# Kernel optimization log

Hardware: AMD Instinct MI355X
Metric: run time of the kernel (lower is better)

## Reference

```python
import jax, jax.numpy as jnp
import numpy as np

D_MODEL = 4096
D_FF = 11008

def setup_inputs() -> dict:
    key = jax.random.key(0)
    k1, k2, k3, k4 = jax.random.split(key, 4)
    x = jax.random.normal(k1, (2, 2048, D_MODEL), dtype=jnp.float32)
    # Linear weights stored torch-style as [out_features, in_features]
    W_gate = jax.random.normal(k2, (D_FF, D_MODEL), dtype=jnp.float32) * (D_MODEL ** -0.5)
    W_up = jax.random.normal(k3, (D_FF, D_MODEL), dtype=jnp.float32) * (D_MODEL ** -0.5)
    W_down = jax.random.normal(k4, (D_MODEL, D_FF), dtype=jnp.float32) * (D_FF ** -0.5)
    return {"x": x, "W_gate": W_gate, "W_up": W_up, "W_down": W_down}

def reference(x, W_gate, W_up, W_down):
    out_shape = x.shape[:-1] + (W_down.shape[0],)
    xf = x.reshape(-1, x.shape[-1])                      # [T, d_model]
    up = jnp.einsum('td,fd->tf', xf, W_up)               # [T, d_ff]
    gate = jax.nn.silu(jnp.einsum('td,fd->tf', xf, W_gate))  # fused SiLU on gate proj
    h = gate * up                                        # [T, d_ff]
    y = jnp.einsum('tf,df->td', h, W_down)               # [T, d_model]
    return y.reshape(out_shape)
```

## Files before the change

kernel.cpp:

```cpp
#include <hip/hip_runtime.h>
#include <hip/hip_bf16.h>

#define D_MODEL 4096
#define D_FF    11008
#define NTOK    4096

typedef __attribute__((ext_vector_type(8))) short short8;
typedef __attribute__((ext_vector_type(4))) float f32x4;

__global__ void k_cvt(const float* __restrict__ in, __hip_bfloat16* __restrict__ out, int n8) {
    int i = blockIdx.x * blockDim.x + threadIdx.x;
    if (i >= n8) return;
    const float4* p = (const float4*)in;
    float4 v0 = p[(size_t)i * 2];
    float4 v1 = p[(size_t)i * 2 + 1];
    float vals[8] = {v0.x, v0.y, v0.z, v0.w, v1.x, v1.y, v1.z, v1.w};
    short8 o;
#pragma unroll
    for (int j = 0; j < 8; ++j) {
        __hip_bfloat16 b = __float2bfloat16(vals[j]);
        o[j] = *reinterpret_cast<short*>(&b);
    }
    *reinterpret_cast<short8*>(out + (size_t)i * 8) = o;
}

static __device__ __forceinline__ void stage_half(
    const __hip_bfloat16* g, int ld, __hip_bfloat16* lds, int tid)
{
#pragma unroll
    for (int s = 0; s < 2; ++s) {
        int ci = s * 512 + tid;
        int r  = ci >> 3;
        int c  = (ci & 7) ^ (r & 7);
        __builtin_amdgcn_global_load_lds(
            (const __attribute__((address_space(1))) void*)(g + (long)r * ld + c * 8),
            (__attribute__((address_space(3))) void*)(lds + ci * 8),
            16, 0, 0);
    }
}

static __device__ __forceinline__ int sw_off(int row, int kb) {
    return row * 64 + ((((kb >> 3) ^ (row & 7))) << 3);
}

#define GEMM_PHASE(cA, cB, IQ, LOADB, STAGE, VMC)                              \
    {                                                                          \
        short8 af[2][2];                                                       \
        _Pragma("unroll")                                                      \
        for (int ii = 0; ii < 2; ++ii)                                         \
            _Pragma("unroll")                                                  \
            for (int kk = 0; kk < 2; ++kk)                                     \
                af[ii][kk] = *reinterpret_cast<const short8*>(                 \
                    &(cA)[sw_off(wm * 128 + ((IQ) * 2 + ii) * 16 + r16,        \
                                 kk * 32 + g4 * 8)]);                          \
        if (LOADB) {                                                           \
            _Pragma("unroll")                                                  \
            for (int kk = 0; kk < 2; ++kk)                                     \
                _Pragma("unroll")                                              \
                for (int j = 0; j < 4; ++j)                                    \
                    bfr[kk][j] = *reinterpret_cast<const short8*>(             \
                        &(cB)[sw_off(wn * 64 + j * 16 + r16,                   \
                                     kk * 32 + g4 * 8)]);                      \
        }                                                                      \
        STAGE;                                                                 \
        VMC;                                                                   \
        __builtin_amdgcn_s_barrier();                                          \
        asm volatile("s_waitcnt lgkmcnt(0)" ::: "memory");                     \
        __builtin_amdgcn_sched_barrier(0);                                     \
        __builtin_amdgcn_s_setprio(1);                                         \
        _Pragma("unroll")                                                      \
        for (int ii = 0; ii < 2; ++ii)                                         \
            _Pragma("unroll")                                                  \
            for (int j = 0; j < 4; ++j) {                                      \
                acc[(IQ) * 2 + ii][j] = __builtin_amdgcn_mfma_f32_16x16x32_bf16( \
                    af[ii][0], bfr[0][j], acc[(IQ) * 2 + ii][j], 0, 0, 0);     \
                acc[(IQ) * 2 + ii][j] = __builtin_amdgcn_mfma_f32_16x16x32_bf16( \
                    af[ii][1], bfr[1][j], acc[(IQ) * 2 + ii][j], 0, 0, 0);     \
            }                                                                  \
        __builtin_amdgcn_s_setprio(0);                                         \
        __builtin_amdgcn_sched_barrier(0);                                     \
        __builtin_amdgcn_s_barrier();                                          \
    }

#define VM4 do { if (pf) asm volatile("s_waitcnt vmcnt(4)" ::: "memory");      \
                 else    asm volatile("s_waitcnt vmcnt(0)" ::: "memory"); } while (0)
#define VMNONE do {} while (0)

template<int EPI>
__global__ __launch_bounds__(512, 2)
void k_gemm(const __hip_bfloat16* __restrict__ A,
            const __hip_bfloat16* __restrict__ B,
            void* __restrict__ C,
            const int M, const int N, const int K, const int nsw)
{
    extern __shared__ __hip_bfloat16 smem[];
    __hip_bfloat16* sA = smem;
    __hip_bfloat16* sB = smem + 32768;

    const int tid  = threadIdx.x;
    const int lane = tid & 63;
    const int wid  = tid >> 6;
    const int wm = wid >> 2, wn = wid & 3;
    const int r16 = lane & 15, g4 = lane >> 4;

    const int bid = blockIdx.x;
    const int o = (bid & 7) * nsw + (bid >> 3);
    const int mt = M >> 8;
    const int n0 = (o / mt) << 8;
    const int m0 = (o % mt) << 8;

    const __hip_bfloat16* Ab = A + (long)m0 * K;
    const __hip_bfloat16* Bb = B + (long)n0 * K;
    const long h1 = (long)128 * K;

    stage_half(Ab,            K, sA + 0,             tid);
    stage_half(Ab + h1,       K, sA + 8192,          tid);
    stage_half(Bb,            K, sB + 0,             tid);
    stage_half(Bb + h1,       K, sB + 8192,          tid);
    stage_half(Bb + 64,       K, sB + 16384,         tid);
    stage_half(Bb + h1 + 64,  K, sB + 16384 + 8192,  tid);
    asm volatile("s_waitcnt vmcnt(4)" ::: "memory");
    __builtin_amdgcn_s_barrier();

    f32x4 acc[8][4];
#pragma unroll
    for (int i = 0; i < 8; ++i)
#pragma unroll
        for (int j = 0; j < 4; ++j)
            acc[i][j] = (f32x4){0.f, 0.f, 0.f, 0.f};

    const int nk = K >> 6;
    const int niter = nk >> 1;

    for (int it = 0; it < niter; ++it) {
        const bool pf = (it + 1 < niter);
        const long ko  = (long)(2 * it + 1) * 64;
        const long kn2 = (long)(2 * it + 2) * 64;
        const long kn3 = (long)(2 * it + 3) * 64;

        {
            const __hip_bfloat16* cA = sA;
            const __hip_bfloat16* cB = sB;
            short8 bfr[2][4];
            GEMM_PHASE(cA, cB, 0, 1,
                stage_half(Ab + ko,      K, sA + 16384,        tid), VMNONE);
            GEMM_PHASE(cA, cB, 1, 0,
                stage_half(Ab + h1 + ko, K, sA + 16384 + 8192, tid), VMNONE);
            GEMM_PHASE(cA, cB, 2, 0,
                if (pf) stage_half(Bb + kn2,      K, sB + 0,    tid), VMNONE);
            GEMM_PHASE(cA, cB, 3, 0,
                if (pf) stage_half(Bb + h1 + kn2, K, sB + 8192, tid), VM4);
        }
        {
            const __hip_bfloat16* cA = sA + 16384;
            const __hip_bfloat16* cB = sB + 16384;
            short8 bfr[2][4];
            GEMM_PHASE(cA, cB, 0, 1,
                if (pf) stage_half(Ab + kn2,      K, sA + 0,    tid), VMNONE);
            GEMM_PHASE(cA, cB, 1, 0,
                if (pf) stage_half(Ab + h1 + kn2, K, sA + 8192, tid), VMNONE);
            GEMM_PHASE(cA, cB, 2, 0,
                if (pf) stage_half(Bb + kn3,      K, sB + 16384, tid), VMNONE);
            GEMM_PHASE(cA, cB, 3, 0,
                if (pf) stage_half(Bb + h1 + kn3, K, sB + 16384 + 8192, tid), VM4);
        }
    }

    float* Cf = (float*)C;
    __hip_bfloat16* Cb = (__hip_bfloat16*)C;
#pragma unroll
    for (int i = 0; i < 8; ++i)
#pragma unroll
        for (int j = 0; j < 4; ++j)
#pragma unroll
            for (int r = 0; r < 4; ++r) {
                long row = m0 + wm * 128 + i * 16 + g4 * 4 + r;
                long col = n0 + wn * 64 + j * 16 + r16;
                float v = acc[i][j][r];
                if (EPI == 0) {
                    float s = v / (1.f + __expf(-v));
                    Cb[row * N + col] = __float2bfloat16(s);
                } else if (EPI == 1) {
                    float gs = __bfloat162float(Cb[row * N + col]);
                    Cb[row * N + col] = __float2bfloat16(gs * v);
                } else {
                    Cf[row * N + col] = v;
                }
            }
}

extern "C" void kernel_launch(void* const* d_in, const int* in_sizes, int n_in,
                              void* d_out, int out_size, void* d_ws, size_t ws_size,
                              hipStream_t stream) {
    const float* x  = (const float*)d_in[0];
    const float* wg = (const float*)d_in[1];
    const float* wu = (const float*)d_in[2];
    const float* wd = (const float*)d_in[3];
    float* y = (float*)d_out;

    char* ws = (char*)d_ws;
    const size_t szX = (size_t)NTOK * D_MODEL * 2;
    const size_t szW = (size_t)D_FF * D_MODEL * 2;
    __hip_bfloat16* Xb  = (__hip_bfloat16*)(ws);
    __hip_bfloat16* Wgb = (__hip_bfloat16*)(ws + szX);
    __hip_bfloat16* Wub = (__hip_bfloat16*)(ws + szX + szW);
    __hip_bfloat16* Wdb = (__hip_bfloat16*)(ws + szX + 2 * szW);
    __hip_bfloat16* Hb  = (__hip_bfloat16*)(ws + szX + 3 * szW);
    (void)ws_size; (void)out_size; (void)n_in; (void)in_sizes;

    const size_t SMEM = 131072;
    hipFuncSetAttribute((const void*)k_gemm<0>, hipFuncAttributeMaxDynamicSharedMemorySize, (int)SMEM);
    hipFuncSetAttribute((const void*)k_gemm<1>, hipFuncAttributeMaxDynamicSharedMemorySize, (int)SMEM);
    hipFuncSetAttribute((const void*)k_gemm<2>, hipFuncAttributeMaxDynamicSharedMemorySize, (int)SMEM);

    const int nX = NTOK * D_MODEL / 8;
    const int nW = D_FF * D_MODEL / 8;
    k_cvt<<<(nX + 255) / 256, 256, 0, stream>>>(x, Xb, nX);
    k_cvt<<<(nW + 255) / 256, 256, 0, stream>>>(wg, Wgb, nW);
    k_cvt<<<(nW + 255) / 256, 256, 0, stream>>>(wu, Wub, nW);
    k_cvt<<<(nW + 255) / 256, 256, 0, stream>>>(wd, Wdb, nW);

    k_gemm<0><<<688, 512, SMEM, stream>>>(Xb, Wgb, (void*)Hb, NTOK, D_FF, D_MODEL, 86);
    k_gemm<1><<<688, 512, SMEM, stream>>>(Xb, Wub, (void*)Hb, NTOK, D_FF, D_MODEL, 86);
    k_gemm<2><<<256, 512, SMEM, stream>>>(Hb, Wdb, (void*)y, NTOK, D_MODEL, D_FF, 32);
}
```

Baseline: 1.144 ms.

## Fuse gate and up projections into one dual-accumulator GEMM kernel

Replaces the two separate gate and up GEMM launches with a single kernel. Each block loads one X tile and matching 128-row tiles of both W_gate and W_up, keeping two accumulator sets. The SiLU(gate)*up product is then written once in the epilogue. This removes the second pass over X, and the read-modify-write of H that the up-projection epilogue used to do. B tiles move to a three-slot LDS ring (160KB LDS per block), which may limit occupancy and changes the pipeline schedule. Both kernels also add an early partial lgkmcnt wait before the barrier.

```diff
diff --git a/kernel.cpp b/kernel.cpp
--- a/kernel.cpp
+++ b/kernel.cpp
@@ -43,7 +43,138 @@
     return row * 64 + ((((kb >> 3) ^ (row & 7))) << 3);
 }
 
-#define GEMM_PHASE(cA, cB, IQ, LOADB, STAGE, VMC)                              \
+
+#define FPHASE(IQ, LOADB, STAGE, VMC)                                          \
+    {                                                                          \
+        short8 af[2][2];                                                       \
+        _Pragma("unroll")                                                      \
+        for (int ii = 0; ii < 2; ++ii)                                         \
+            _Pragma("unroll")                                                  \
+            for (int kk = 0; kk < 2; ++kk)                                     \
+                af[ii][kk] = *reinterpret_cast<const short8*>(                 \
+                    &cA[sw_off(wm * 128 + ((IQ) * 2 + ii) * 16 + r16,          \
+                               kk * 32 + g4 * 8)]);                            \
+        if (LOADB) {                                                           \
+            _Pragma("unroll")                                                  \
+            for (int kk = 0; kk < 2; ++kk)                                     \
+                _Pragma("unroll")                                              \
+                for (int j = 0; j < 2; ++j) {                                  \
+                    bg[kk][j] = *reinterpret_cast<const short8*>(              \
+                        &cB[sw_off(wn * 32 + j * 16 + r16, kk * 32 + g4 * 8)]); \
+                    bu[kk][j] = *reinterpret_cast<const short8*>(              \
+                        &cB[8192 + sw_off(wn * 32 + j * 16 + r16, kk * 32 + g4 * 8)]); \
+                }                                                              \
+        }                                                                      \
+        STAGE;                                                                 \
+        VMC;                                                                   \
+        if (LOADB) asm volatile("s_waitcnt lgkmcnt(8)" ::: "memory");          \
+        __builtin_amdgcn_s_barrier();                                          \
+        asm volatile("s_waitcnt lgkmcnt(0)" ::: "memory");                     \
+        __builtin_amdgcn_sched_barrier(0);                                     \
+        __builtin_amdgcn_s_setprio(1);                                         \
+        _Pragma("unroll")                                                      \
+        for (int ii = 0; ii < 2; ++ii)                                         \
+            _Pragma("unroll")                                                  \
+            for (int j = 0; j < 2; ++j) {                                      \
+                accg[(IQ) * 2 + ii][j] = __builtin_amdgcn_mfma_f32_16x16x32_bf16( \
+                    af[ii][0], bg[0][j], accg[(IQ) * 2 + ii][j], 0, 0, 0);     \
+                accg[(IQ) * 2 + ii][j] = __builtin_amdgcn_mfma_f32_16x16x32_bf16( \
+                    af[ii][1], bg[1][j], accg[(IQ) * 2 + ii][j], 0, 0, 0);     \
+                accu[(IQ) * 2 + ii][j] = __builtin_amdgcn_mfma_f32_16x16x32_bf16( \
+                    af[ii][0], bu[0][j], accu[(IQ) * 2 + ii][j], 0, 0, 0);     \
+                accu[(IQ) * 2 + ii][j] = __builtin_amdgcn_mfma_f32_16x16x32_bf16( \
+                    af[ii][1], bu[1][j], accu[(IQ) * 2 + ii][j], 0, 0, 0);     \
+            }                                                                  \
+        __builtin_amdgcn_s_setprio(0);                                         \
+        __builtin_amdgcn_sched_barrier(0);                                     \
+        __builtin_amdgcn_s_barrier();                                          \
+    }
+
+__global__ __launch_bounds__(512, 2)
+void k_gateup(const __hip_bfloat16* __restrict__ X,
+              const __hip_bfloat16* __restrict__ Wg,
+              const __hip_bfloat16* __restrict__ Wu,
+              __hip_bfloat16* __restrict__ H)
+{
+    extern __shared__ __hip_bfloat16 smem[];
+    __hip_bfloat16* sA = smem;
+    __hip_bfloat16* sB = smem + 32768;
+
+    const int tid  = threadIdx.x;
+    const int lane = tid & 63;
+    const int wid  = tid >> 6;
+    const int wm = wid >> 2, wn = wid & 3;
+    const int r16 = lane & 15, g4 = lane >> 4;
+
+    const int bid = blockIdx.x;
+    const int o = (bid & 7) * 172 + (bid >> 3);
+    const int n0 = (o >> 4) * 128;
+    const int m0 = (o & 15) * 256;
+
+    const int K = D_MODEL;
+    const __hip_bfloat16* Ab = X  + (long)m0 * K;
+    const __hip_bfloat16* Gb = Wg + (long)n0 * K;
+    const __hip_bfloat16* Ub = Wu + (long)n0 * K;
+    const long h1 = (long)128 * K;
+
+    stage_half(Ab,           K, sA + 0,              tid);
+    stage_half(Ab + h1,      K, sA + 8192,           tid);
+    stage_half(Gb,           K, sB + 0,              tid);
+    stage_half(Ub,           K, sB + 8192,           tid);
+    stage_half(Gb + 64,      K, sB + 16384,          tid);
+    stage_half(Ub + 64,      K, sB + 16384 + 8192,   tid);
+    asm volatile("s_waitcnt vmcnt(4)" ::: "memory");
+    __builtin_amdgcn_s_barrier();
+
+    f32x4 accg[8][2], accu[8][2];
+#pragma unroll
+    for (int i = 0; i < 8; ++i)
+#pragma unroll
+        for (int j = 0; j < 2; ++j) {
+            accg[i][j] = (f32x4){0.f, 0.f, 0.f, 0.f};
+            accu[i][j] = (f32x4){0.f, 0.f, 0.f, 0.f};
+        }
+
+    const int nk = K >> 6;
+    int rb = 0;
+    for (int t = 0; t < nk; ++t) {
+        const __hip_bfloat16* cA = sA + (t & 1) * 16384;
+        const __hip_bfloat16* cB = sB + rb * 16384;
+        __hip_bfloat16* nA = sA + ((t & 1) ^ 1) * 16384;
+        int wb = rb + 2; if (wb >= 3) wb -= 3;
+        __hip_bfloat16* wB = sB + wb * 16384;
+        const bool pf1 = (t + 1 < nk);
+        const bool pf2 = (t + 2 < nk);
+        const long kc1 = (long)(t + 1) * 64;
+        const long kc2 = (long)(t + 2) * 64;
+        short8 bg[2][2], bu[2][2];
+
+        FPHASE(0, 1, if (pf1) stage_half(Ab + kc1,      K, nA,        tid), );
+        FPHASE(1, 0, if (pf1) stage_half(Ab + h1 + kc1, K, nA + 8192, tid), );
+        FPHASE(2, 0, if (pf2) stage_half(Gb + kc2,      K, wB,        tid), );
+        FPHASE(3, 0, if (pf2) stage_half(Ub + kc2,      K, wB + 8192, tid),
+               do { if (pf2) asm volatile("s_waitcnt vmcnt(4)" ::: "memory");
+                    else     asm volatile("s_waitcnt vmcnt(0)" ::: "memory"); } while (0));
+
+        rb = rb + 1; if (rb >= 3) rb -= 3;
+    }
+
+#pragma unroll
+    for (int i = 0; i < 8; ++i)
+#pragma unroll
+        for (int j = 0; j < 2; ++j)
+#pragma unroll
+            for (int r = 0; r < 4; ++r) {
+                long row = m0 + wm * 128 + i * 16 + g4 * 4 + r;
+                long col = n0 + wn * 32 + j * 16 + r16;
+                float g = accg[i][j][r];
+                float u = accu[i][j][r];
+                float s = g / (1.f + __expf(-g));
+                H[row * D_FF + col] = __float2bfloat16(s * u);
+            }
+}
+
+#define DPHASE(cA, cB, IQ, LOADB, STAGE, VMC)                                  \
     {                                                                          \
         short8 af[2][2];                                                       \
         _Pragma("unroll")                                                      \
@@ -64,6 +195,7 @@
         }                                                                      \
         STAGE;                                                                 \
         VMC;                                                                   \
+        if (LOADB) asm volatile("s_waitcnt lgkmcnt(8)" ::: "memory");          \
         __builtin_amdgcn_s_barrier();                                          \
         asm volatile("s_waitcnt lgkmcnt(0)" ::: "memory");                     \
         __builtin_amdgcn_sched_barrier(0);                                     \
@@ -82,16 +214,13 @@
         __builtin_amdgcn_s_barrier();                                          \
     }
 
-#define VM4 do { if (pf) asm volatile("s_waitcnt vmcnt(4)" ::: "memory");      \
-                 else    asm volatile("s_waitcnt vmcnt(0)" ::: "memory"); } while (0)
-#define VMNONE do {} while (0)
-
-template<int EPI>
+#define VM4D do { if (pf) asm volatile("s_waitcnt vmcnt(4)" ::: "memory");     \
+                  else    asm volatile("s_waitcnt vmcnt(0)" ::: "memory"); } while (0)
+
 __global__ __launch_bounds__(512, 2)
-void k_gemm(const __hip_bfloat16* __restrict__ A,
+void k_down(const __hip_bfloat16* __restrict__ A,
             const __hip_bfloat16* __restrict__ B,
-            void* __restrict__ C,
-            const int M, const int N, const int K, const int nsw)
+            float* __restrict__ Y)
 {
     extern __shared__ __hip_bfloat16 smem[];
     __hip_bfloat16* sA = smem;
@@ -104,11 +233,12 @@
     const int r16 = lane & 15, g4 = lane >> 4;
 
     const int bid = blockIdx.x;
-    const int o = (bid & 7) * nsw + (bid >> 3);
-    const int mt = M >> 8;
-    const int n0 = (o / mt) << 8;
-    const int m0 = (o % mt) << 8;
-
+    const int o = (bid & 7) * 32 + (bid >> 3);
+    const int n0 = (o >> 4) << 8;
+    const int m0 = (o & 15) << 8;
+
+    const int K = D_FF;
+    const int N = D_MODEL;
     const __hip_bfloat16* Ab = A + (long)m0 * K;
     const __hip_bfloat16* Bb = B + (long)n0 * K;
     const long h1 = (long)128 * K;
@@ -137,37 +267,34 @@
         const long ko  = (long)(2 * it + 1) * 64;
         const long kn2 = (long)(2 * it + 2) * 64;
         const long kn3 = (long)(2 * it + 3) * 64;
-
         {
             const __hip_bfloat16* cA = sA;
             const __hip_bfloat16* cB = sB;
             short8 bfr[2][4];
-            GEMM_PHASE(cA, cB, 0, 1,
-                stage_half(Ab + ko,      K, sA + 16384,        tid), VMNONE);
-            GEMM_PHASE(cA, cB, 1, 0,
-                stage_half(Ab + h1 + ko, K, sA + 16384 + 8192, tid), VMNONE);
-            GEMM_PHASE(cA, cB, 2, 0,
-                if (pf) stage_half(Bb + kn2,      K, sB + 0,    tid), VMNONE);
-            GEMM_PHASE(cA, cB, 3, 0,
-                if (pf) stage_half(Bb + h1 + kn2, K, sB + 8192, tid), VM4);
+            DPHASE(cA, cB, 0, 1,
+                stage_half(Ab + ko,      K, sA + 16384,        tid), );
+            DPHASE(cA, cB, 1, 0,
+                stage_half(Ab + h1 + ko, K, sA + 16384 + 8192, tid), );
+            DPHASE(cA, cB, 2, 0,
+                if (pf) stage_half(Bb + kn2,      K, sB + 0,    tid), );
+            DPHASE(cA, cB, 3, 0,
+                if (pf) stage_half(Bb + h1 + kn2, K, sB + 8192, tid), VM4D);
         }
         {
             const __hip_bfloat16* cA = sA + 16384;
             const __hip_bfloat16* cB = sB + 16384;
             short8 bfr[2][4];
-            GEMM_PHASE(cA, cB, 0, 1,
-                if (pf) stage_half(Ab + kn2,      K, sA + 0,    tid), VMNONE);
-            GEMM_PHASE(cA, cB, 1, 0,
-                if (pf) stage_half(Ab + h1 + kn2, K, sA + 8192, tid), VMNONE);
-            GEMM_PHASE(cA, cB, 2, 0,
-                if (pf) stage_half(Bb + kn3,      K, sB + 16384, tid), VMNONE);
-            GEMM_PHASE(cA, cB, 3, 0,
-                if (pf) stage_half(Bb + h1 + kn3, K, sB + 16384 + 8192, tid), VM4);
+            DPHASE(cA, cB, 0, 1,
+                if (pf) stage_half(Ab + kn2,      K, sA + 0,    tid), );
+            DPHASE(cA, cB, 1, 0,
+                if (pf) stage_half(Ab + h1 + kn2, K, sA + 8192, tid), );
+            DPHASE(cA, cB, 2, 0,
+                if (pf) stage_half(Bb + kn3,      K, sB + 16384, tid), );
+            DPHASE(cA, cB, 3, 0,
+                if (pf) stage_half(Bb + h1 + kn3, K, sB + 16384 + 8192, tid), VM4D);
         }
     }
 
-    float* Cf = (float*)C;
-    __hip_bfloat16* Cb = (__hip_bfloat16*)C;
 #pragma unroll
     for (int i = 0; i < 8; ++i)
 #pragma unroll
@@ -176,16 +303,7 @@
             for (int r = 0; r < 4; ++r) {
                 long row = m0 + wm * 128 + i * 16 + g4 * 4 + r;
                 long col = n0 + wn * 64 + j * 16 + r16;
-                float v = acc[i][j][r];
-                if (EPI == 0) {
-                    float s = v / (1.f + __expf(-v));
-                    Cb[row * N + col] = __float2bfloat16(s);
-                } else if (EPI == 1) {
-                    float gs = __bfloat162float(Cb[row * N + col]);
-                    Cb[row * N + col] = __float2bfloat16(gs * v);
-                } else {
-                    Cf[row * N + col] = v;
-                }
+                Y[row * N + col] = acc[i][j][r];
             }
 }
 
@@ -208,10 +326,10 @@
     __hip_bfloat16* Hb  = (__hip_bfloat16*)(ws + szX + 3 * szW);
     (void)ws_size; (void)out_size; (void)n_in; (void)in_sizes;
 
-    const size_t SMEM = 131072;
-    hipFuncSetAttribute((const void*)k_gemm<0>, hipFuncAttributeMaxDynamicSharedMemorySize, (int)SMEM);
-    hipFuncSetAttribute((const void*)k_gemm<1>, hipFuncAttributeMaxDynamicSharedMemorySize, (int)SMEM);
-    hipFuncSetAttribute((const void*)k_gemm<2>, hipFuncAttributeMaxDynamicSharedMemorySize, (int)SMEM);
+    const int SMEM_GU = 163840;
+    const int SMEM_D  = 131072;
+    hipFuncSetAttribute((const void*)k_gateup, hipFuncAttributeMaxDynamicSharedMemorySize, SMEM_GU);
+    hipFuncSetAttribute((const void*)k_down,   hipFuncAttributeMaxDynamicSharedMemorySize, SMEM_D);
 
     const int nX = NTOK * D_MODEL / 8;
     const int nW = D_FF * D_MODEL / 8;
@@ -220,7 +338,6 @@
     k_cvt<<<(nW + 255) / 256, 256, 0, stream>>>(wu, Wub, nW);
     k_cvt<<<(nW + 255) / 256, 256, 0, stream>>>(wd, Wdb, nW);
 
-    k_gemm<0><<<688, 512, SMEM, stream>>>(Xb, Wgb, (void*)Hb, NTOK, D_FF, D_MODEL, 86);
-    k_gemm<1><<<688, 512, SMEM, stream>>>(Xb, Wub, (void*)Hb, NTOK, D_FF, D_MODEL, 86);
-    k_gemm<2><<<256, 512, SMEM, stream>>>(Hb, Wdb, (void*)y, NTOK, D_MODEL, D_FF, 32);
-}
+    k_gateup<<<1376, 512, SMEM_GU, stream>>>(Xb, Wgb, Wub, Hb);
+    k_down<<<256, 512, SMEM_D, stream>>>(Hb, Wdb, y);
+}
```

New measurement: 1.068 ms. 6.7% less time.

## Overlap W_down fp32-to-bf16 conversion with up-projection GEMM via extra blocks

Applied to the files above, without the earlier changes.

The standalone conversion kernel for W_down is removed. Instead, 160 extra workgroups are appended to the up-projection GEMM launch, and they perform that conversion while the GEMM workgroups run. This aims to fill idle CU slots (688 GEMM blocks do not fill the device evenly) and to drop one kernel launch. The change also adds a partial lgkmcnt wait before the barrier in B-loading phases, and passes niter and tile-index math as constants or shifts instead of deriving them in the kernel. The risk is that the conversion blocks compete with the GEMM for memory bandwidth.

```diff
diff --git a/kernel.cpp b/kernel.cpp
--- a/kernel.cpp
+++ b/kernel.cpp
@@ -38,12 +38,15 @@
             16, 0, 0);
     }
 }
-
 static __device__ __forceinline__ int sw_off(int row, int kb) {
     return row * 64 + ((((kb >> 3) ^ (row & 7))) << 3);
 }
 
-#define GEMM_PHASE(cA, cB, IQ, LOADB, STAGE, VMC)                              \
+#define MFMA16(a, b, c) __builtin_amdgcn_mfma_f32_16x16x32_bf16(a, b, c, 0, 0, 0)
+#define VM4D do { if (pf) asm volatile("s_waitcnt vmcnt(4)" ::: "memory");     \
+                  else    asm volatile("s_waitcnt vmcnt(0)" ::: "memory"); } while (0)
+
+#define DPHASE(cA, cB, IQ, LOADB, STAGE, VMC)                                  \
     {                                                                          \
         short8 af[2][2];                                                       \
         _Pragma("unroll")                                                      \
@@ -64,6 +67,7 @@
         }                                                                      \
         STAGE;                                                                 \
         VMC;                                                                   \
+        if (LOADB) asm volatile("s_waitcnt lgkmcnt(8)" ::: "memory");          \
         __builtin_amdgcn_s_barrier();                                          \
         asm volatile("s_waitcnt lgkmcnt(0)" ::: "memory");                     \
         __builtin_amdgcn_sched_barrier(0);                                     \
@@ -72,42 +76,58 @@
         for (int ii = 0; ii < 2; ++ii)                                         \
             _Pragma("unroll")                                                  \
             for (int j = 0; j < 4; ++j) {                                      \
-                acc[(IQ) * 2 + ii][j] = __builtin_amdgcn_mfma_f32_16x16x32_bf16( \
-                    af[ii][0], bfr[0][j], acc[(IQ) * 2 + ii][j], 0, 0, 0);     \
-                acc[(IQ) * 2 + ii][j] = __builtin_amdgcn_mfma_f32_16x16x32_bf16( \
-                    af[ii][1], bfr[1][j], acc[(IQ) * 2 + ii][j], 0, 0, 0);     \
+                acc[(IQ) * 2 + ii][j] = MFMA16(af[ii][0], bfr[0][j],           \
+                                               acc[(IQ) * 2 + ii][j]);         \
+                acc[(IQ) * 2 + ii][j] = MFMA16(af[ii][1], bfr[1][j],           \
+                                               acc[(IQ) * 2 + ii][j]);         \
             }                                                                  \
         __builtin_amdgcn_s_setprio(0);                                         \
         __builtin_amdgcn_sched_barrier(0);                                     \
         __builtin_amdgcn_s_barrier();                                          \
     }
-
-#define VM4 do { if (pf) asm volatile("s_waitcnt vmcnt(4)" ::: "memory");      \
-                 else    asm volatile("s_waitcnt vmcnt(0)" ::: "memory"); } while (0)
-#define VMNONE do {} while (0)
 
 template<int EPI>
 __global__ __launch_bounds__(512, 2)
 void k_gemm(const __hip_bfloat16* __restrict__ A,
             const __hip_bfloat16* __restrict__ B,
             void* __restrict__ C,
-            const int M, const int N, const int K, const int nsw)
+            const int K, const int niter, const int nout, const int nsw,
+            const int ngemm,
+            const float* __restrict__ Wd32, __hip_bfloat16* __restrict__ Wdb)
 {
     extern __shared__ __hip_bfloat16 smem[];
     __hip_bfloat16* sA = smem;
     __hip_bfloat16* sB = smem + 32768;
 
-    const int tid  = threadIdx.x;
+    const int tid = threadIdx.x;
+    const int bid = blockIdx.x;
+
+    if (bid >= ngemm) {
+        const long total8 = (long)D_MODEL * D_FF / 8;
+        const long stride = 160L * 512;
+        for (long i = (long)(bid - ngemm) * 512 + tid; i < total8; i += stride) {
+            const float4* p = (const float4*)(Wd32 + i * 8);
+            float4 v0 = p[0], v1 = p[1];
+            float vals[8] = {v0.x, v0.y, v0.z, v0.w, v1.x, v1.y, v1.z, v1.w};
+            short8 oo;
+#pragma unroll
+            for (int j = 0; j < 8; ++j) {
+                __hip_bfloat16 b = __float2bfloat16(vals[j]);
+                oo[j] = *reinterpret_cast<short*>(&b);
+            }
+            *reinterpret_cast<short8*>(Wdb + i * 8) = oo;
+        }
+        return;
+    }
+
     const int lane = tid & 63;
     const int wid  = tid >> 6;
     const int wm = wid >> 2, wn = wid & 3;
     const int r16 = lane & 15, g4 = lane >> 4;
 
-    const int bid = blockIdx.x;
     const int o = (bid & 7) * nsw + (bid >> 3);
-    const int mt = M >> 8;
-    const int n0 = (o / mt) << 8;
-    const int m0 = (o % mt) << 8;
+    const int n0 = (o >> 4) << 8;
+    const int m0 = (o & 15) << 8;
 
     const __hip_bfloat16* Ab = A + (long)m0 * K;
     const __hip_bfloat16* Bb = B + (long)n0 * K;
@@ -129,40 +149,36 @@
         for (int j = 0; j < 4; ++j)
             acc[i][j] = (f32x4){0.f, 0.f, 0.f, 0.f};
 
-    const int nk = K >> 6;
-    const int niter = nk >> 1;
-
     for (int it = 0; it < niter; ++it) {
         const bool pf = (it + 1 < niter);
         const long ko  = (long)(2 * it + 1) * 64;
         const long kn2 = (long)(2 * it + 2) * 64;
         const long kn3 = (long)(2 * it + 3) * 64;
-
         {
             const __hip_bfloat16* cA = sA;
             const __hip_bfloat16* cB = sB;
             short8 bfr[2][4];
-            GEMM_PHASE(cA, cB, 0, 1,
-                stage_half(Ab + ko,      K, sA + 16384,        tid), VMNONE);
-            GEMM_PHASE(cA, cB, 1, 0,
-                stage_half(Ab + h1 + ko, K, sA + 16384 + 8192, tid), VMNONE);
-            GEMM_PHASE(cA, cB, 2, 0,
-                if (pf) stage_half(Bb + kn2,      K, sB + 0,    tid), VMNONE);
-            GEMM_PHASE(cA, cB, 3, 0,
-                if (pf) stage_half(Bb + h1 + kn2, K, sB + 8192, tid), VM4);
+            DPHASE(cA, cB, 0, 1,
+                stage_half(Ab + ko,      K, sA + 16384,        tid), );
+            DPHASE(cA, cB, 1, 0,
+                stage_half(Ab + h1 + ko, K, sA + 16384 + 8192, tid), );
+            DPHASE(cA, cB, 2, 0,
+                if (pf) stage_half(Bb + kn2,      K, sB + 0,    tid), );
+            DPHASE(cA, cB, 3, 0,
+                if (pf) stage_half(Bb + h1 + kn2, K, sB + 8192, tid), VM4D);
         }
         {
             const __hip_bfloat16* cA = sA + 16384;
             const __hip_bfloat16* cB = sB + 16384;
             short8 bfr[2][4];
-            GEMM_PHASE(cA, cB, 0, 1,
-                if (pf) stage_half(Ab + kn2,      K, sA + 0,    tid), VMNONE);
-            GEMM_PHASE(cA, cB, 1, 0,
-                if (pf) stage_half(Ab + h1 + kn2, K, sA + 8192, tid), VMNONE);
-            GEMM_PHASE(cA, cB, 2, 0,
-                if (pf) stage_half(Bb + kn3,      K, sB + 16384, tid), VMNONE);
-            GEMM_PHASE(cA, cB, 3, 0,
-                if (pf) stage_half(Bb + h1 + kn3, K, sB + 16384 + 8192, tid), VM4);
+            DPHASE(cA, cB, 0, 1,
+                if (pf) stage_half(Ab + kn2,      K, sA + 0,    tid), );
+            DPHASE(cA, cB, 1, 0,
+                if (pf) stage_half(Ab + h1 + kn2, K, sA + 8192, tid), );
+            DPHASE(cA, cB, 2, 0,
+                if (pf) stage_half(Bb + kn3,      K, sB + 16384, tid), );
+            DPHASE(cA, cB, 3, 0,
+                if (pf) stage_half(Bb + h1 + kn3, K, sB + 16384 + 8192, tid), VM4D);
         }
     }
 
@@ -179,12 +195,12 @@
                 float v = acc[i][j][r];
                 if (EPI == 0) {
                     float s = v / (1.f + __expf(-v));
-                    Cb[row * N + col] = __float2bfloat16(s);
+                    Cb[row * nout + col] = __float2bfloat16(s);
                 } else if (EPI == 1) {
-                    float gs = __bfloat162float(Cb[row * N + col]);
-                    Cb[row * N + col] = __float2bfloat16(gs * v);
+                    float gs = __bfloat162float(Cb[row * nout + col]);
+                    Cb[row * nout + col] = __float2bfloat16(gs * v);
                 } else {
-                    Cf[row * N + col] = v;
+                    Cf[row * nout + col] = v;
                 }
             }
 }
@@ -208,19 +224,21 @@
     __hip_bfloat16* Hb  = (__hip_bfloat16*)(ws + szX + 3 * szW);
     (void)ws_size; (void)out_size; (void)n_in; (void)in_sizes;
 
-    const size_t SMEM = 131072;
-    hipFuncSetAttribute((const void*)k_gemm<0>, hipFuncAttributeMaxDynamicSharedMemorySize, (int)SMEM);
-    hipFuncSetAttribute((const void*)k_gemm<1>, hipFuncAttributeMaxDynamicSharedMemorySize, (int)SMEM);
-    hipFuncSetAttribute((const void*)k_gemm<2>, hipFuncAttributeMaxDynamicSharedMemorySize, (int)SMEM);
+    const int SMEM = 131072;
+    hipFuncSetAttribute((const void*)k_gemm<0>, hipFuncAttributeMaxDynamicSharedMemorySize, SMEM);
+    hipFuncSetAttribute((const void*)k_gemm<1>, hipFuncAttributeMaxDynamicSharedMemorySize, SMEM);
+    hipFuncSetAttribute((const void*)k_gemm<2>, hipFuncAttributeMaxDynamicSharedMemorySize, SMEM);
 
     const int nX = NTOK * D_MODEL / 8;
     const int nW = D_FF * D_MODEL / 8;
+
     k_cvt<<<(nX + 255) / 256, 256, 0, stream>>>(x, Xb, nX);
     k_cvt<<<(nW + 255) / 256, 256, 0, stream>>>(wg, Wgb, nW);
+    k_gemm<0><<<688, 512, SMEM, stream>>>(Xb, Wgb, (void*)Hb,
+        D_MODEL, 32, D_FF, 86, 688, nullptr, nullptr);
     k_cvt<<<(nW + 255) / 256, 256, 0, stream>>>(wu, Wub, nW);
-    k_cvt<<<(nW + 255) / 256, 256, 0, stream>>>(wd, Wdb, nW);
-
-    k_gemm<0><<<688, 512, SMEM, stream>>>(Xb, Wgb, (void*)Hb, NTOK, D_FF, D_MODEL, 86);
-    k_gemm<1><<<688, 512, SMEM, stream>>>(Xb, Wub, (void*)Hb, NTOK, D_FF, D_MODEL, 86);
-    k_gemm<2><<<256, 512, SMEM, stream>>>(Hb, Wdb, (void*)y, NTOK, D_MODEL, D_FF, 32);
-}
+    k_gemm<1><<<848, 512, SMEM, stream>>>(Xb, Wub, (void*)Hb,
+        D_MODEL, 32, D_FF, 86, 688, wd, Wdb);
+    k_gemm<2><<<256, 512, SMEM, stream>>>(Hb, Wdb, (void*)y,
+        D_FF, 86, D_MODEL, 32, 256, nullptr, nullptr);
+}
```

Measured after the change: 1.130 ms. About the same (-1.2%).
